# Optimization experiments

Hardware: AMD Instinct MI355X
Metric: run time of the kernel (lower is better)

## Reference

```python
import jax, jax.numpy as jnp
import numpy as np

B, S, H = 1, 4096, 2048
HQ, HKV, D = 8, 4, 256
WIN = 1024          # sliding window
SOFTCAP = 50.0      # attn logit softcapping
EPS = 1e-6          # rms_norm_eps
ROPE_THETA = 10000.0


def setup_inputs() -> dict:
    key = jax.random.key(0)
    ks = jax.random.split(key, 6)
    hidden_states = jax.random.normal(ks[0], (B, S, H), dtype=jnp.float32)
    # RoPE cos/sin tables, shape [B, S, D]
    inv_freq = 1.0 / (ROPE_THETA ** (jnp.arange(0, D, 2, dtype=jnp.float32) / D))
    pos = jnp.arange(S, dtype=jnp.float32)
    freqs = pos[:, None] * inv_freq[None, :]          # [S, D/2]
    emb = jnp.concatenate([freqs, freqs], axis=-1)    # [S, D]
    cos = jnp.broadcast_to(jnp.cos(emb)[None], (B, S, D)).astype(jnp.float32)
    sin = jnp.broadcast_to(jnp.sin(emb)[None], (B, S, D)).astype(jnp.float32)
    qpos = jnp.arange(S)[:, None]
    kpos = jnp.arange(S)[None, :]
    diff = qpos - kpos
    allowed = (diff >= 0) & (diff < WIN)
    attention_mask = jnp.where(allowed, 0.0, -1e9).astype(jnp.float32)[None, None]
    attention_mask = jnp.broadcast_to(attention_mask, (B, 1, S, S))
    w_scale = 0.02
    Wq = jax.random.normal(ks[1], (HQ * D, H), dtype=jnp.float32) * w_scale
    Wk = jax.random.normal(ks[2], (HKV * D, H), dtype=jnp.float32) * w_scale
    Wv = jax.random.normal(ks[3], (HKV * D, H), dtype=jnp.float32) * w_scale
    Wo = jax.random.normal(ks[4], (H, HQ * D), dtype=jnp.float32) * w_scale
    q_norm_w = jnp.ones((D,), dtype=jnp.float32)
    k_norm_w = jnp.ones((D,), dtype=jnp.float32)
    return {"hidden_states": hidden_states, "cos": cos, "sin": sin,
            "attention_mask": attention_mask, "Wq": Wq, "Wk": Wk, "Wv": Wv,
            "Wo": Wo, "q_norm_w": q_norm_w, "k_norm_w": k_norm_w}


def _rms_norm(x, weight=None):
    # Gemma4 RMSNorm in fp32: x * rsqrt(mean(x^2) + eps) [* weight]
    ms = jnp.mean(x * x, axis=-1, keepdims=True) + EPS
    y = x * jax.lax.rsqrt(ms)
    return y * weight if weight is not None else y


def _rope(x, cos, sin):
    # x: [B,S,Hn,D]; cos/sin: [B,S,D] -> unsqueeze at dim 2
    x1, x2 = jnp.split(x, 2, axis=-1)
    rot = jnp.concatenate([-x2, x1], axis=-1)
    return x * cos[:, :, None, :] + rot * sin[:, :, None, :]


def reference(hidden_states, cos, sin, attention_mask, Wq, Wk, Wv, Wo, q_norm_w, k_norm_w):
    n_rep = HQ // HKV
    q = (hidden_states @ Wq.T).reshape(B, S, HQ, D)     # [B,S,HQ,D]
    q = _rms_norm(q, q_norm_w)
    q = _rope(q, cos, sin).transpose(0, 2, 1, 3)        # [B,HQ,S,D]
    k = (hidden_states @ Wk.T).reshape(B, S, HKV, D)
    k = _rms_norm(k, k_norm_w)
    k = _rope(k, cos, sin).transpose(0, 2, 1, 3)        # [B,HKV,S,D]
    v = (hidden_states @ Wv.T).reshape(B, S, HKV, D)
    v = _rms_norm(v).transpose(0, 2, 1, 3)              # [B,HKV,S,D]
    # repeat_kv (GQA)
    k = jnp.repeat(k, n_rep, axis=1)                    # [B,HQ,S,D]
    v = jnp.repeat(v, n_rep, axis=1)
    scores = jnp.einsum('bhqd,bhkd->bhqk', q, k)        # scaling = 1.0
    scores = jnp.tanh(scores / SOFTCAP) * SOFTCAP       # softcap
    scores = scores + attention_mask
    attn = jax.nn.softmax(scores.astype(jnp.float32), axis=-1).astype(q.dtype)
    out = jnp.einsum('bhqk,bhkd->bhqd', attn, v)        # [B,HQ,S,D]
    out = out.transpose(0, 2, 1, 3).reshape(B, S, HQ * D)
    return out @ Wo.T                                   # [B,S,H]
```

## Files before the change

kernel.cpp:

```cpp
#include <hip/hip_runtime.h>

#define S_LEN 4096
#define HID   2048
#define NHQ   8
#define NKV   4
#define DHEAD 256
#define WIN   1024

typedef __attribute__((ext_vector_type(4))) float     floatx4;
typedef __attribute__((ext_vector_type(8))) _Float16  halfx8;
typedef __attribute__((ext_vector_type(8))) __bf16    bf16x8;

__device__ __forceinline__ unsigned short f2h(float f){
  union { _Float16 h; unsigned short u; } cv; cv.h = (_Float16)f; return cv.u;
}
__device__ __forceinline__ float h2f(unsigned short u){
  union { unsigned short u; _Float16 h; } cv; cv.u = u; return (float)cv.h;
}
__device__ __forceinline__ unsigned short f2bf(float f){
  unsigned int u = __float_as_uint(f);
  u += 0x7FFFu + ((u >> 16) & 1u);
  return (unsigned short)(u >> 16);
}

__device__ __forceinline__ void gld_lds16(const void* g, void* l){
  __builtin_amdgcn_global_load_lds((const __attribute__((address_space(1))) void*)g,
                                   (__attribute__((address_space(3))) void*)l, 16, 0, 0);
}

__global__ __launch_bounds__(256) void cvt_all(const float* __restrict__ hs,
                                               const float* __restrict__ Wq,
                                               const float* __restrict__ Wk,
                                               const float* __restrict__ Wv,
                                               const float* __restrict__ Wo,
                                               unsigned short* __restrict__ h_h,
                                               unsigned short* __restrict__ w_qkv,
                                               unsigned short* __restrict__ wo){
  int bid = blockIdx.x;
  const float* src;
  unsigned short* dst;
  size_t i;
  if (bid < 8192){
    i = ((size_t)bid * 256 + threadIdx.x) * 4;
    src = hs + i; dst = h_h + i;
  } else if (bid < 16384){
    i = ((size_t)(bid - 8192) * 256 + threadIdx.x) * 4;
    int row = (int)(i >> 11), col = (int)(i & 2047);
    src = ((row < 2048) ? (Wq + ((size_t)row << 11))
         : (row < 3072) ? (Wk + ((size_t)(row - 2048) << 11))
                        : (Wv + ((size_t)(row - 3072) << 11))) + col;
    dst = w_qkv + i;
  } else {
    i = ((size_t)(bid - 16384) * 256 + threadIdx.x) * 4;
    src = Wo + i; dst = wo + i;
  }
  float4 v = *(const float4*)src;
  *(ushort4*)dst = make_ushort4(f2h(v.x), f2h(v.y), f2h(v.z), f2h(v.w));
}

template<int OUT_F32>
__global__ __launch_bounds__(256, 2) void gemm_cnt(const unsigned short* __restrict__ A,
                                                   const unsigned short* __restrict__ B,
                                                   void* __restrict__ Cv,
                                                   int ldC, int K, int nx){
  __shared__ __align__(16) unsigned short As[2][128 * 64];
  __shared__ __align__(16) unsigned short Bs[2][128 * 64];
  const int T = K >> 6;
  const int t0 = threadIdx.x, w = t0 >> 6, lane = t0 & 63;
  const int wm = w >> 1, wn = w & 1;
  const int quad = lane >> 4, l15 = lane & 15;

  const int bid = (int)blockIdx.x;
  const int rgx = nx >> 3;
  const int gen = bid >> 9;
  const int rr  = bid & 511;
  const int xcd = rr & 7;
  const int k8  = rr >> 3;
  const int rby = xcd / rgx, rbx = xcd - rby * rgx;
  const int by  = gen * ((8 / rgx) << 3) + (rby << 3) + (k8 >> 3);
  const int bx  = (rbx << 3) + (k8 & 7);
  const int bm0 = by * 128, bn0 = bx * 128;

  const int grow = lane >> 3;
  const int sg8  = (((lane & 7) ^ grow) << 3);

#define STG(U, SL) {                                                          \
    _Pragma("unroll")                                                         \
    for (int j = 0; j < 4; ++j){                                              \
      const int ch = w + 4 * j;                                               \
      const int gr = ch * 8 + grow;                                           \
      gld_lds16(A + (size_t)(bm0 + gr) * K + (size_t)(U) * 64 + sg8,          \
                &As[SL][ch * 512]);                                           \
      gld_lds16(B + (size_t)(bn0 + gr) * K + (size_t)(U) * 64 + sg8,          \
                &Bs[SL][ch * 512]);                                           \
    } }

  STG(0, 0)

  const floatx4 zf = {0.f, 0.f, 0.f, 0.f};
  floatx4 acc[4][4];
#pragma unroll
  for (int mi = 0; mi < 4; ++mi)
#pragma unroll
    for (int ni = 0; ni < 4; ++ni) acc[mi][ni] = zf;

  for (int t = 0; t < T; ++t){
    const int cur = t & 1;
    if (t + 1 < T){
      STG(t + 1, cur ^ 1)
      asm volatile("s_waitcnt vmcnt(8)" ::: "memory");
    } else {
      asm volatile("s_waitcnt vmcnt(0)" ::: "memory");
    }
    __builtin_amdgcn_s_barrier();
    __builtin_amdgcn_sched_barrier(0);

    halfx8 af[4][2], bf[4][2];
#pragma unroll
    for (int mi = 0; mi < 4; ++mi){
      const int r = wm * 64 + mi * 16 + l15;
      const int s0 = (quad ^ (r & 7)) << 3;
      af[mi][0] = *(const halfx8*)&As[cur][r * 64 + s0];
      af[mi][1] = *(const halfx8*)&As[cur][r * 64 + (s0 ^ 32)];
    }
#pragma unroll
    for (int ni = 0; ni < 4; ++ni){
      const int r = wn * 64 + ni * 16 + l15;
      const int s0 = (quad ^ (r & 7)) << 3;
      bf[ni][0] = *(const halfx8*)&Bs[cur][r * 64 + s0];
      bf[ni][1] = *(const halfx8*)&Bs[cur][r * 64 + (s0 ^ 32)];
    }
    asm volatile("s_waitcnt lgkmcnt(8)" ::: "memory");
    __builtin_amdgcn_sched_barrier(0);
    __builtin_amdgcn_s_setprio(1);
#pragma unroll
    for (int mi = 0; mi < 4; ++mi)
#pragma unroll
      for (int ni = 0; ni < 4; ++ni)
        acc[mi][ni] = __builtin_amdgcn_mfma_f32_16x16x32_f16(af[mi][0], bf[ni][0], acc[mi][ni], 0, 0, 0);
    __builtin_amdgcn_s_setprio(0);
    asm volatile("s_waitcnt lgkmcnt(0)" ::: "memory");
    __builtin_amdgcn_sched_barrier(0);
    __builtin_amdgcn_s_setprio(1);
#pragma unroll
    for (int mi = 0; mi < 4; ++mi)
#pragma unroll
      for (int ni = 0; ni < 4; ++ni)
        acc[mi][ni] = __builtin_amdgcn_mfma_f32_16x16x32_f16(af[mi][1], bf[ni][1], acc[mi][ni], 0, 0, 0);
    __builtin_amdgcn_s_setprio(0);
    __builtin_amdgcn_s_barrier();
    __builtin_amdgcn_sched_barrier(0);
  }
#undef STG

#pragma unroll
  for (int mi = 0; mi < 4; ++mi)
#pragma unroll
    for (int ni = 0; ni < 4; ++ni)
#pragma unroll
      for (int r = 0; r < 4; ++r){
        int m = bm0 + wm*64 + mi*16 + quad*4 + r;
        int n = bn0 + wn*64 + ni*16 + l15;
        float v = acc[mi][ni][r];
        if (OUT_F32) ((float*)Cv)[(size_t)m * ldC + n] = v;
        else         ((unsigned short*)Cv)[(size_t)m * ldC + n] = f2h(v);
      }
}

__global__ __launch_bounds__(256) void qkv_post(const unsigned short* __restrict__ qkvh,
                                                const float* __restrict__ cosb,
                                                const float* __restrict__ sinb,
                                                const float* __restrict__ qnw,
                                                const float* __restrict__ knw,
                                                unsigned short* __restrict__ Qf,
                                                unsigned short* __restrict__ Kf,
                                                unsigned short* __restrict__ Vf){
  int gw   = blockIdx.x * 4 + (threadIdx.x >> 6);
  int lane = threadIdx.x & 63;
  int hh = gw & 15, s = gw >> 4;
  int colbase = (hh < 8) ? hh * 256 : (hh < 12 ? 2048 + (hh - 8) * 256 : 3072 + (hh - 12) * 256);

  ushort4 raw = *(const ushort4*)(qkvh + (size_t)s * 4096 + colbase + lane * 4);
  float x0 = h2f(raw.x), x1 = h2f(raw.y), x2 = h2f(raw.z), x3 = h2f(raw.w);
  float ss = x0*x0 + x1*x1 + x2*x2 + x3*x3;
#pragma unroll
  for (int off = 32; off; off >>= 1) ss += __shfl_xor(ss, off);
  float inv = rsqrtf(ss * (1.0f / 256.0f) + 1e-6f);

  if (hh < 12){
    const float* wp = (hh < 8) ? qnw : knw;
    float4 wv = *(const float4*)(wp + lane * 4);
    float y[4] = { x0*inv*wv.x, x1*inv*wv.y, x2*inv*wv.z, x3*inv*wv.w };
    float4 cv = *(const float4*)(cosb + (size_t)s * 256 + lane * 4);
    float4 sv = *(const float4*)(sinb + (size_t)s * 256 + lane * 4);
    float cj[4] = {cv.x, cv.y, cv.z, cv.w};
    float sj[4] = {sv.x, sv.y, sv.z, sv.w};
    unsigned short oh[4];
#pragma unroll
    for (int j = 0; j < 4; ++j){
      float oth = __shfl_xor(y[j], 32);
      float rot = (lane < 32) ? -oth : oth;
      oh[j] = f2h(y[j] * cj[j] + rot * sj[j]);
    }
    ushort4 r = make_ushort4(oh[0], oh[1], oh[2], oh[3]);
    if (hh < 8) *(ushort4*)(Qf + (size_t)(hh       * S_LEN + s) * DHEAD + lane * 4) = r;
    else        *(ushort4*)(Kf + (size_t)((hh - 8) * S_LEN + s) * DHEAD + lane * 4) = r;
  } else {
    ushort4 r = make_ushort4(f2bf(x0*inv), f2bf(x1*inv), f2bf(x2*inv), f2bf(x3*inv));
    *(ushort4*)(Vf + (size_t)((hh - 12) * S_LEN + s) * DHEAD + lane * 4) = r;
  }
}

__global__ __launch_bounds__(256) void transpose_v(const unsigned short* __restrict__ v,
                                                   unsigned short* __restrict__ vt){
  __shared__ unsigned short tile[64][68];
  int kv = blockIdx.z, d0 = blockIdx.x * 64, s0 = blockIdx.y * 64;
  int t = threadIdx.x;
  int r = t >> 4, c4 = (t & 15) * 4;
#pragma unroll
  for (int i = 0; i < 4; ++i){
    int row = r + i * 16;
    ushort4 xx = *(const ushort4*)(v + (size_t)(kv * S_LEN + s0 + row) * DHEAD + d0 + c4);
    tile[row][c4] = xx.x; tile[row][c4+1] = xx.y; tile[row][c4+2] = xx.z; tile[row][c4+3] = xx.w;
  }
  __syncthreads();
#pragma unroll
  for (int i = 0; i < 4; ++i){
    int dr = r + i * 16;
    ushort4 yy = make_ushort4(tile[c4][dr], tile[c4+1][dr], tile[c4+2][dr], tile[c4+3][dr]);
    *(ushort4*)(vt + (size_t)(kv * DHEAD + d0 + dr) * S_LEN + s0 + c4) = yy;
  }
}

__global__ __launch_bounds__(512, 2) void attn_win(const unsigned short* __restrict__ Qg,
                                                   const unsigned short* __restrict__ Kg,
                                                   const unsigned short* __restrict__ Vt,
                                                   unsigned short* __restrict__ Og){
  __shared__ __align__(16) unsigned short Ks[2][8 * 32 * 32];
  __shared__ __align__(16) unsigned short Vts[2][256 * 32];
  __shared__ __align__(16) unsigned short Pb[8][16 * 40];

  const int bid = blockIdx.x;
  const int h = bid & 7, kv = h >> 1;
  const int q0 = (bid >> 3) * 128;
  const int t = threadIdx.x, w = t >> 6, lane = t & 63;
  const int quad = lane >> 4, l15 = lane & 15;
  const int l2 = lane >> 2;
  const int gsw = (((lane & 3) ^ ((l2 >> 1) & 3)) << 3);
  const int qsw = ((quad ^ ((l15 >> 1) & 3)) << 3);
  const int qw0 = q0 + w * 16;

  halfx8 qf[8];
#pragma unroll
  for (int c = 0; c < 8; ++c)
    qf[c] = *(const halfx8*)(Qg + (size_t)(h * S_LEN + qw0 + l15) * DHEAD + c*32 + quad*8);

  const floatx4 zf = {0.f, 0.f, 0.f, 0.f};
  floatx4 oacc[16];
#pragma unroll
  for (int dt = 0; dt < 16; ++dt) oacc[dt] = zf;
  float l_part[4] = {0.f, 0.f, 0.f, 0.f};

  int kt_lo = q0 / 32 - 32; if (kt_lo < 0) kt_lo = 0;
  int kt_hi = q0 / 32 + 3;

  const size_t kbase = (size_t)kv * S_LEN * DHEAD;
  const size_t vbase = (size_t)kv * DHEAD * S_LEN;

#define STAGE(KT, B)                                                              \
  {                                                                               \
    const int key0_ = (KT) * 32;                                                  \
    _Pragma("unroll")                                                             \
    for (int j = 0; j < 2; ++j){                                                  \
      int ch = j * 8 + w;                                                         \
      int krow = (ch & 1) * 16 + l2;                                              \
      int cb = ch >> 1;                                                           \
      gld_lds16(Kg + kbase + (size_t)(key0_ + krow) * DHEAD + cb * 32 + gsw,      \
                &Ks[B][ch * 512]);                                                \
      int drow = ch * 16 + l2;                                                    \
      gld_lds16(Vt + vbase + (size_t)drow * S_LEN + key0_ + gsw,                  \
                &Vts[B][ch * 512]);                                               \
    }                                                                             \
  }

  STAGE(kt_lo, 0);

  for (int kt = kt_lo; kt <= kt_hi; ++kt){
    const int cur = (kt - kt_lo) & 1;
    if (kt < kt_hi){
      STAGE(kt + 1, cur ^ 1);
      asm volatile("s_waitcnt vmcnt(4)" ::: "memory");
    } else {
      asm volatile("s_waitcnt vmcnt(0)" ::: "memory");
    }
    __builtin_amdgcn_s_barrier();

    const int key0 = kt * 32;
    if (key0 <= qw0 + 15 && key0 + 31 >= qw0 - (WIN - 1)){
      floatx4 sc[2];
      sc[0] = zf; sc[1] = zf;
      __builtin_amdgcn_s_setprio(1);
#pragma unroll
      for (int c = 0; c < 8; ++c){
#pragma unroll
        for (int nt = 0; nt < 2; ++nt){
          halfx8 kf = *(const halfx8*)&Ks[cur][c * 1024 + (nt*16 + l15) * 32 + qsw];
          sc[nt] = __builtin_amdgcn_mfma_f32_16x16x32_f16(qf[c], kf, sc[nt], 0, 0, 0);
        }
      }
      __builtin_amdgcn_s_setprio(0);
      const bool tfull = (key0 + 31 <= qw0) && (qw0 + 15 - key0 < WIN);
#pragma unroll
      for (int nt = 0; nt < 2; ++nt)
#pragma unroll
        for (int r = 0; r < 4; ++r){
          float v = sc[nt][r];
          float e  = __builtin_amdgcn_exp2f(v * 0.0577078016f);
          float tt = __builtin_amdgcn_rcpf(e + 1.0f);
          float p  = __builtin_amdgcn_exp2f(fmaf(tt, -144.26950408f, 28.8539008f));
          if (!tfull){
            int qi = qw0 + quad*4 + r;
            int ki = key0 + nt*16 + l15;
            p = ((ki <= qi) && (qi - ki < WIN)) ? p : 0.0f;
          }
          l_part[r] += p;
          Pb[w][(quad*4 + r) * 40 + nt*16 + l15] = f2bf(p);
        }
      bf16x8 pf = *(const bf16x8*)&Pb[w][l15 * 40 + quad * 8];
      __builtin_amdgcn_s_setprio(1);
#pragma unroll
      for (int dt = 0; dt < 16; ++dt){
        bf16x8 vf = *(const bf16x8*)&Vts[cur][(dt*16 + l15) * 32 + qsw];
        oacc[dt] = __builtin_amdgcn_mfma_f32_16x16x32_bf16(pf, vf, oacc[dt], 0, 0, 0);
      }
      __builtin_amdgcn_s_setprio(0);
    }
    __builtin_amdgcn_s_barrier();
  }
#undef STAGE

#pragma unroll
  for (int r = 0; r < 4; ++r){
    float l = l_part[r];
    l += __shfl_xor(l, 1);
    l += __shfl_xor(l, 2);
    l += __shfl_xor(l, 4);
    l += __shfl_xor(l, 8);
    float rl = 1.0f / l;
    int srow = qw0 + quad*4 + r;
#pragma unroll
    for (int dt = 0; dt < 16; ++dt)
      Og[(size_t)srow * (NHQ * DHEAD) + h * DHEAD + dt*16 + l15] = f2h(oacc[dt][r] * rl);
  }
}

extern "C" void kernel_launch(void* const* d_in, const int* in_sizes, int n_in,
                              void* d_out, int out_size, void* d_ws, size_t ws_size,
                              hipStream_t stream){
  const float* hs   = (const float*)d_in[0];
  const float* cosb = (const float*)d_in[1];
  const float* sinb = (const float*)d_in[2];
  const float* Wq   = (const float*)d_in[4];
  const float* Wk   = (const float*)d_in[5];
  const float* Wv   = (const float*)d_in[6];
  const float* Wo   = (const float*)d_in[7];
  const float* qnw  = (const float*)d_in[8];
  const float* knw  = (const float*)d_in[9];
  float* out = (float*)d_out;

  const size_t MB = 1024ull * 1024ull;
  char* ws = (char*)d_ws;
  unsigned short* h_h   = (unsigned short*)(ws);
  unsigned short* w_qkv = (unsigned short*)(ws + 16 * MB);
  unsigned short* wo    = (unsigned short*)(ws + 32 * MB);
  unsigned short* qkvh  = (unsigned short*)(ws + 40 * MB);
  unsigned short* Qf    = (unsigned short*)(ws);
  unsigned short* Kf    = (unsigned short*)(ws + 16 * MB);
  unsigned short* Vf    = (unsigned short*)(ws + 24 * MB);
  unsigned short* vt    = (unsigned short*)(ws + 40 * MB);
  unsigned short* ob    = (unsigned short*)(ws + 48 * MB);

  cvt_all<<<20480, 256, 0, stream>>>(hs, Wq, Wk, Wv, Wo, h_h, w_qkv, wo);

  gemm_cnt<0><<<1024, 256, 0, stream>>>(h_h, w_qkv, qkvh, 4096, 2048, 32);

  qkv_post<<<16384, 256, 0, stream>>>(qkvh, cosb, sinb, qnw, knw, Qf, Kf, Vf);
  transpose_v<<<dim3(4, 64, 4), 256, 0, stream>>>(Vf, vt);

  attn_win<<<256, 512, 0, stream>>>(Qf, Kf, vt, ob);

  gemm_cnt<1><<<512, 256, 0, stream>>>(ob, wo, out, 2048, 2048, 16);
}
```

Before: 383.6 us.

## Replace QKV projection GEMM with 256x256-tile 8-wave pipelined kernel

Adds a new GEMM kernel for the QKV projection that uses 256x256 output tiles with 8 waves (512 threads) instead of 128x128 tiles with 4 waves. K-tile loads for the next step are split into four quarters, each interleaved with one quarter of the MFMA work, and s_setprio raises priority around the MFMA bursts. The larger tile raises arithmetic intensity and cuts global reloads of A and B. In exchange it uses 128 KB of LDS and a large accumulator array, launches only 256 blocks, and drops the XCD-aware block remapping the old kernel used.

```diff
diff --git a/kernel.cpp b/kernel.cpp
--- a/kernel.cpp
+++ b/kernel.cpp
@@ -58,6 +58,145 @@
   *(ushort4*)dst = make_ushort4(f2h(v.x), f2h(v.y), f2h(v.z), f2h(v.w));
 }
 
+__global__ __launch_bounds__(512, 2) void gemm_qkv8(const unsigned short* __restrict__ A,
+                                                    const unsigned short* __restrict__ B,
+                                                    unsigned short* __restrict__ C,
+                                                    int ldC, int K, int nx){
+  __shared__ __align__(16) unsigned short As[2][256 * 64];
+  __shared__ __align__(16) unsigned short Bs[2][256 * 64];
+  const int T = K >> 6;
+  const int t0 = threadIdx.x, w = t0 >> 6, lane = t0 & 63;
+  const int wm = w >> 2, wn = w & 3;
+  const int quad = lane >> 4, l15 = lane & 15;
+  const int r7 = l15 & 7;
+
+  const int bid = (int)blockIdx.x;
+  const int by = bid / nx, bx = bid - by * nx;
+  const int bm0 = by * 256, bn0 = bx * 256;
+
+  const int grow = lane >> 3;
+  const int sg8  = (((lane & 7) ^ grow) << 3);
+
+#define STGH(U, HALF)                                                          \
+  {                                                                            \
+    const int sl_ = (U) & 1;                                                   \
+    const unsigned short* src_ = ((HALF) < 2)                                  \
+        ? (A + (size_t)(bm0 + (((HALF) & 1) << 7)) * K)                        \
+        : (B + (size_t)(bn0 + (((HALF) & 1) << 7)) * K);                       \
+    unsigned short* dst_ = (((HALF) < 2) ? &As[sl_][0] : &Bs[sl_][0])          \
+                           + ((((HALF) & 1) << 7) * 64);                       \
+    _Pragma("unroll")                                                          \
+    for (int L = 0; L < 2; ++L){                                               \
+      const int ck = L * 8 + w;                                                \
+      gld_lds16(src_ + (size_t)((ck << 3) + grow) * K + (size_t)(U) * 64 + sg8,\
+                dst_ + ck * 512);                                              \
+    }                                                                          \
+  }
+
+#define LDA(MI, KS) (*(const halfx8*)&Ap[(wm*128 + (MI)*16 + l15) * 64 + ((((KS)*4 + quad) ^ r7) << 3)])
+#define LDB(NI, KS) (*(const halfx8*)&Bp[(wn*64  + (NI)*16 + l15) * 64 + ((((KS)*4 + quad) ^ r7) << 3)])
+
+  STGH(0, 0) STGH(0, 1) STGH(0, 2) STGH(0, 3)
+  asm volatile("s_waitcnt vmcnt(0)" ::: "memory");
+  __builtin_amdgcn_s_barrier();
+
+  const floatx4 zf = {0.f, 0.f, 0.f, 0.f};
+  floatx4 acc[8][4];
+#pragma unroll
+  for (int mi = 0; mi < 8; ++mi)
+#pragma unroll
+    for (int ni = 0; ni < 4; ++ni) acc[mi][ni] = zf;
+
+  for (int t = 0; t < T; ++t){
+    const int cur = t & 1;
+    const unsigned short* Ap = &As[cur][0];
+    const unsigned short* Bp = &Bs[cur][0];
+    const bool pf = (t + 1 < T);
+    halfx8 af[4], bf0[4], bf1[4];
+
+#pragma unroll
+    for (int mi = 0; mi < 4; ++mi) af[mi] = LDA(mi, 0);
+#pragma unroll
+    for (int ni = 0; ni < 4; ++ni){ bf0[ni] = LDB(ni, 0); bf1[ni] = LDB(ni, 1); }
+    if (pf) STGH(t + 1, 0)
+    __builtin_amdgcn_s_barrier();
+    asm volatile("s_waitcnt lgkmcnt(0)" ::: "memory");
+    __builtin_amdgcn_sched_barrier(0);
+    __builtin_amdgcn_s_setprio(1);
+#pragma unroll
+    for (int mi = 0; mi < 4; ++mi)
+#pragma unroll
+      for (int ni = 0; ni < 4; ++ni)
+        acc[mi][ni] = __builtin_amdgcn_mfma_f32_16x16x32_f16(af[mi], bf0[ni], acc[mi][ni], 0, 0, 0);
+    __builtin_amdgcn_s_setprio(0);
+    __builtin_amdgcn_s_barrier();
+    __builtin_amdgcn_sched_barrier(0);
+
+#pragma unroll
+    for (int mi = 0; mi < 4; ++mi) af[mi] = LDA(4 + mi, 0);
+    if (pf) STGH(t + 1, 1)
+    __builtin_amdgcn_s_barrier();
+    asm volatile("s_waitcnt lgkmcnt(0)" ::: "memory");
+    __builtin_amdgcn_sched_barrier(0);
+    __builtin_amdgcn_s_setprio(1);
+#pragma unroll
+    for (int mi = 0; mi < 4; ++mi)
+#pragma unroll
+      for (int ni = 0; ni < 4; ++ni)
+        acc[4 + mi][ni] = __builtin_amdgcn_mfma_f32_16x16x32_f16(af[mi], bf0[ni], acc[4 + mi][ni], 0, 0, 0);
+    __builtin_amdgcn_s_setprio(0);
+    __builtin_amdgcn_s_barrier();
+    __builtin_amdgcn_sched_barrier(0);
+
+#pragma unroll
+    for (int mi = 0; mi < 4; ++mi) af[mi] = LDA(mi, 1);
+    if (pf) STGH(t + 1, 2)
+    __builtin_amdgcn_s_barrier();
+    asm volatile("s_waitcnt lgkmcnt(0)" ::: "memory");
+    __builtin_amdgcn_sched_barrier(0);
+    __builtin_amdgcn_s_setprio(1);
+#pragma unroll
+    for (int mi = 0; mi < 4; ++mi)
+#pragma unroll
+      for (int ni = 0; ni < 4; ++ni)
+        acc[mi][ni] = __builtin_amdgcn_mfma_f32_16x16x32_f16(af[mi], bf1[ni], acc[mi][ni], 0, 0, 0);
+    __builtin_amdgcn_s_setprio(0);
+    __builtin_amdgcn_s_barrier();
+    __builtin_amdgcn_sched_barrier(0);
+
+#pragma unroll
+    for (int mi = 0; mi < 4; ++mi) af[mi] = LDA(4 + mi, 1);
+    if (pf) STGH(t + 1, 3)
+    __builtin_amdgcn_s_barrier();
+    asm volatile("s_waitcnt lgkmcnt(0)" ::: "memory");
+    __builtin_amdgcn_sched_barrier(0);
+    __builtin_amdgcn_s_setprio(1);
+#pragma unroll
+    for (int mi = 0; mi < 4; ++mi)
+#pragma unroll
+      for (int ni = 0; ni < 4; ++ni)
+        acc[4 + mi][ni] = __builtin_amdgcn_mfma_f32_16x16x32_f16(af[mi], bf1[ni], acc[4 + mi][ni], 0, 0, 0);
+    __builtin_amdgcn_s_setprio(0);
+    if (pf) { asm volatile("s_waitcnt vmcnt(0)" ::: "memory"); }
+    __builtin_amdgcn_s_barrier();
+    __builtin_amdgcn_sched_barrier(0);
+  }
+#undef STGH
+#undef LDA
+#undef LDB
+
+#pragma unroll
+  for (int mi = 0; mi < 8; ++mi)
+#pragma unroll
+    for (int ni = 0; ni < 4; ++ni)
+#pragma unroll
+      for (int r = 0; r < 4; ++r){
+        int m = bm0 + wm*128 + mi*16 + quad*4 + r;
+        int n = bn0 + wn*64 + ni*16 + l15;
+        C[(size_t)m * ldC + n] = f2h(acc[mi][ni][r]);
+      }
+}
+
 template<int OUT_F32>
 __global__ __launch_bounds__(256, 2) void gemm_cnt(const unsigned short* __restrict__ A,
                                                    const unsigned short* __restrict__ B,
@@ -382,7 +521,7 @@
 
   cvt_all<<<20480, 256, 0, stream>>>(hs, Wq, Wk, Wv, Wo, h_h, w_qkv, wo);
 
-  gemm_cnt<0><<<1024, 256, 0, stream>>>(h_h, w_qkv, qkvh, 4096, 2048, 32);
+  gemm_qkv8<<<256, 512, 0, stream>>>(h_h, w_qkv, qkvh, 4096, 2048, 16);
 
   qkv_post<<<16384, 256, 0, stream>>>(qkvh, cosb, sinb, qnw, knw, Qf, Kf, Vf);
   transpose_v<<<dim3(4, 64, 4), 256, 0, stream>>>(Vf, vt);
```

Result: faster. 370.9 us (-3.3%).
